# Optimization experiments

Hardware: AMD Instinct MI355X
Metric: run time of the kernel (lower is better)

The kernel has to match this reference:

```python
import jax, jax.numpy as jnp
import numpy as np

EPS = 1e-8  # torch.cosine_similarity default eps


def setup_inputs() -> dict:
    key = jax.random.key(0)
    ks = jax.random.split(key, 6)
    B, U, P, H = 256, 128, 64, 768
    utt_output = jax.random.normal(ks[0], (U, B, H), dtype=jnp.float32)
    pheno_output = jax.random.normal(ks[1], (P, B, H), dtype=jnp.float32)
    # Conv1d(in=U, out=U, kernel=P) weight: [out, in, kernel]
    w_utt = jax.random.normal(ks[2], (U, U, P), dtype=jnp.float32) / np.sqrt(U * P)
    b_utt = jax.random.normal(ks[3], (U,), dtype=jnp.float32) * 0.01
    # Conv1d(in=P, out=P, kernel=U) weight: [out, in, kernel]
    w_pheno = jax.random.normal(ks[4], (P, P, U), dtype=jnp.float32) / np.sqrt(P * U)
    b_pheno = jax.random.normal(ks[5], (P,), dtype=jnp.float32) * 0.01
    return {"utt_output": utt_output, "pheno_output": pheno_output,
            "w_utt": w_utt, "b_utt": b_utt, "w_pheno": w_pheno, "b_pheno": b_pheno}


def reference(utt_output, pheno_output, w_utt, b_utt, w_pheno, b_pheno):
    # [len, B, H] -> [B, len, H]
    u = jnp.swapaxes(utt_output, 0, 1)    # [B, U, H]
    p = jnp.swapaxes(pheno_output, 0, 1)  # [B, P, H]
    # cosine similarity matrix c[b,i,j] = <u_i, p_j> / (max(|u_i|,eps)*max(|p_j|,eps))
    un = u / jnp.maximum(jnp.linalg.norm(u, axis=-1, keepdims=True), EPS)
    pn = p / jnp.maximum(jnp.linalg.norm(p, axis=-1, keepdims=True), EPS)
    c = jnp.einsum('buh,bph->bup', un, pn)  # [B, U, P]
    # Conv1d with kernel covering the full width -> output length 1, i.e. an einsum
    row_logits = jnp.einsum('bup,oup->bo', c, w_utt) + b_utt        # [B, U]
    col_logits = jnp.einsum('bup,opu->bo', c, w_pheno) + b_pheno    # [B, P]
    row_attention = jax.nn.softmax(row_logits, axis=-1)
    col_attention = jax.nn.softmax(col_logits, axis=-1)
    return row_attention, col_attention
```

## Files before the change

### kernel.cpp

```cpp
#include <hip/hip_runtime.h>
#include <stdint.h>

#define Bn 256
#define Un 128
#define Pn 64
#define Hn 768
#define Ototal 192
#define KC 16

#define LDU 40
#define LDB 72

typedef short s4v __attribute__((ext_vector_type(4)));
typedef short s8v __attribute__((ext_vector_type(8)));
typedef float f4v __attribute__((ext_vector_type(4)));

__device__ __forceinline__ short f2bf(float x) {
  union { float f; uint32_t u; } c; c.f = x;
  uint32_t r = (c.u + 0x7fffu + ((c.u >> 16) & 1u)) >> 16;
  return (short)(r & 0xffffu);
}

__device__ __forceinline__ float dot4(float4 v) {
  return v.x * v.x + v.y * v.y + v.z * v.z + v.w * v.w;
}

__global__ void __launch_bounds__(512) phaseAW(const float* __restrict__ utt,
                                               const float* __restrict__ ph,
                                               ushort* __restrict__ Cbf,
                                               const float* __restrict__ w_utt,
                                               const float* __restrict__ w_ph,
                                               ushort* __restrict__ Wbf) {
  __shared__ __align__(16) float smemf[64 * 129];
  char* smem = (char*)smemf;
  const int bx = blockIdx.x;
  const int t = threadIdx.x;

  if (bx >= 512) {
    if (bx < 2560) {
      int idx = (bx - 512) * 512 + t;
      Wbf[idx] = (ushort)f2bf(w_utt[idx]);
      return;
    }
    float* tile = smemf;
    const int oc = bx - 2560;
    const float* src = w_ph + (size_t)oc * 8192;
#pragma unroll
    for (int itr = 0; itr < 4; ++itr) {
      int idx = itr * 2048 + t * 4;
      int j = idx >> 7, i = idx & 127;
      float4 v = *(const float4*)(src + idx);
      tile[j * 129 + i + 0] = v.x;
      tile[j * 129 + i + 1] = v.y;
      tile[j * 129 + i + 2] = v.z;
      tile[j * 129 + i + 3] = v.w;
    }
    __syncthreads();
    const size_t obase = (size_t)(128 + oc) * 8192;
#pragma unroll
    for (int itr = 0; itr < 4; ++itr) {
      int k = itr * 2048 + t * 4;
      int i = k >> 6, j = k & 63;
      s4v o4 = { f2bf(tile[(j + 0) * 129 + i]),
                 f2bf(tile[(j + 1) * 129 + i]),
                 f2bf(tile[(j + 2) * 129 + i]),
                 f2bf(tile[(j + 3) * 129 + i]) };
      *(s4v*)&Wbf[obase + k] = o4;
    }
    return;
  }

  short (*uA)[64 * LDU] = (short (*)[64 * LDU])(smem);
  short (*pB)[64 * LDU] = (short (*)[64 * LDU])(smem + 10240);
  float* s_inu = (float*)(smem + 20480);
  float* s_inp = (float*)(smem + 20736);

  const int b    = (bx & 7) | ((bx >> 4) << 3);
  const int half = (bx >> 3) & 1;
  const int w = t >> 6, l = t & 63;

  const int r  = t >> 3;
  const int cc = (t & 7) * 4;

  const size_t rstride = (size_t)Bn * Hn;
  const float* ubase = utt + (size_t)b * Hn + (size_t)(half * 64 + r) * rstride + cc;
  const float* pbase = ph  + (size_t)b * Hn + (size_t)r * rstride + cc;

  const int m  = l & 15;
  const int ko = (l >> 4) * 8;
  const int it = w & 3;
  const int jp = w >> 2;
  const int lw = r * LDU + (t & 7) * 4;
  const int fo = (it * 16 + m) * LDU + ko;
  const int go = (jp * 32 + m) * LDU + ko;

  f4v zero4 = {0.f, 0.f, 0.f, 0.f};
  f4v acc0 = zero4, acc1 = zero4;
  float ssu = 0.f, ssp = 0.f;

  float4 pu[4], pp[4];
  pu[0] = *(const float4*)(ubase);
  pp[0] = *(const float4*)(pbase);
  pu[1] = *(const float4*)(ubase + 32);
  pp[1] = *(const float4*)(pbase + 32);
  pu[2] = *(const float4*)(ubase + 64);
  pp[2] = *(const float4*)(pbase + 64);
  pu[3] = *(const float4*)(ubase + 96);
  pp[3] = *(const float4*)(pbase + 96);

  {
    float4 a = pu[0], q = pp[0];
    ssu += dot4(a); ssp += dot4(q);
    s4v au = { f2bf(a.x), f2bf(a.y), f2bf(a.z), f2bf(a.w) };
    s4v qq = { f2bf(q.x), f2bf(q.y), f2bf(q.z), f2bf(q.w) };
    *(s4v*)&uA[0][lw] = au;
    *(s4v*)&pB[0][lw] = qq;
  }
  asm volatile("s_waitcnt lgkmcnt(0)" ::: "memory");
  __builtin_amdgcn_s_barrier();
  __builtin_amdgcn_sched_barrier(0);

#pragma unroll
  for (int c = 0; c < 24; ++c) {
    const int cur = c & 1;
    if (c + 4 < 24) {
      pu[(c + 4) & 3] = *(const float4*)(ubase + (c + 4) * 32);
      pp[(c + 4) & 3] = *(const float4*)(pbase + (c + 4) * 32);
    }
    s8v af  = *(const s8v*)&uA[cur][fo];
    s8v bf0 = *(const s8v*)&pB[cur][go];
    s8v bf1 = *(const s8v*)&pB[cur][go + 16 * LDU];
    acc0 = __builtin_amdgcn_mfma_f32_16x16x32_bf16(af, bf0, acc0, 0, 0, 0);
    acc1 = __builtin_amdgcn_mfma_f32_16x16x32_bf16(af, bf1, acc1, 0, 0, 0);
    if (c + 1 < 24) {
      float4 a = pu[(c + 1) & 3], q = pp[(c + 1) & 3];
      ssu += dot4(a); ssp += dot4(q);
      s4v au = { f2bf(a.x), f2bf(a.y), f2bf(a.z), f2bf(a.w) };
      s4v qq = { f2bf(q.x), f2bf(q.y), f2bf(q.z), f2bf(q.w) };
      *(s4v*)&uA[cur ^ 1][lw] = au;
      *(s4v*)&pB[cur ^ 1][lw] = qq;
    }
    asm volatile("s_waitcnt lgkmcnt(0)" ::: "memory");
    __builtin_amdgcn_s_barrier();
    __builtin_amdgcn_sched_barrier(0);
  }

  ssu += __shfl_xor(ssu, 4); ssu += __shfl_xor(ssu, 2); ssu += __shfl_xor(ssu, 1);
  ssp += __shfl_xor(ssp, 4); ssp += __shfl_xor(ssp, 2); ssp += __shfl_xor(ssp, 1);
  if ((t & 7) == 0) {
    s_inu[r] = 1.f / fmaxf(sqrtf(ssu), 1e-8f);
    s_inp[r] = 1.f / fmaxf(sqrtf(ssp), 1e-8f);
  }
  __syncthreads();

  const int cl = l & 15;
  const int rq = (l >> 4) * 4;
#pragma unroll
  for (int jt = 0; jt < 2; ++jt) {
    int j = jp * 32 + jt * 16 + cl;
    float sj = s_inp[j];
    f4v a = (jt == 0) ? acc0 : acc1;
#pragma unroll
    for (int rr = 0; rr < 4; ++rr) {
      int il = it * 16 + rq + rr;
      float v = a[rr] * s_inu[il] * sj;
      Cbf[((size_t)b * Un + half * 64 + il) * Pn + j] = (ushort)f2bf(v);
    }
  }
}

__global__ void __launch_bounds__(256) phaseB(const ushort* __restrict__ Cbf,
                                              const ushort* __restrict__ Wbf,
                                              float* __restrict__ partial) {
  const int kc = blockIdx.x;
  const int mt = blockIdx.y;
  const int nt = blockIdx.z;
  const int t = threadIdx.x;
  const int w = t >> 6, l = t & 63;

  __shared__ short Ab[64 * LDB];
  __shared__ short Bb[64 * LDB];

  const int row = t >> 2;
  const int k16 = (t & 3) * 16;

  f4v zero4 = {0.f, 0.f, 0.f, 0.f};
  f4v acc[4] = {zero4, zero4, zero4, zero4};

  const ushort* Ag = Cbf + (size_t)(mt * 64 + row) * 8192 + kc * 512 + k16;
  const ushort* Bg = Wbf + (size_t)(nt * 64 + row) * 8192 + kc * 512 + k16;
  const int m  = l & 15;
  const int ko = (l >> 4) * 8;

  for (int c = 0; c < 8; ++c) {
    s8v av0 = *(const s8v*)(Ag + c * 64);
    s8v av1 = *(const s8v*)(Ag + c * 64 + 8);
    s8v bv0 = *(const s8v*)(Bg + c * 64);
    s8v bv1 = *(const s8v*)(Bg + c * 64 + 8);
    __syncthreads();
    *(s8v*)&Ab[row * LDB + k16]     = av0;
    *(s8v*)&Ab[row * LDB + k16 + 8] = av1;
    *(s8v*)&Bb[row * LDB + k16]     = bv0;
    *(s8v*)&Bb[row * LDB + k16 + 8] = bv1;
    __syncthreads();
#pragma unroll
    for (int ks = 0; ks < 2; ++ks) {
      s8v af = *(const s8v*)&Ab[(16 * w + m) * LDB + ks * 32 + ko];
#pragma unroll
      for (int jt = 0; jt < 4; ++jt) {
        s8v bf = *(const s8v*)&Bb[(16 * jt + m) * LDB + ks * 32 + ko];
        acc[jt] = __builtin_amdgcn_mfma_f32_16x16x32_bf16(af, bf, acc[jt], 0, 0, 0);
      }
    }
  }

  const int rq = (l >> 4) * 4;
#pragma unroll
  for (int jt = 0; jt < 4; ++jt) {
    int og = nt * 64 + 16 * jt + (l & 15);
#pragma unroll
    for (int r = 0; r < 4; ++r) {
      int bg = mt * 64 + 16 * w + rq + r;
      partial[((size_t)kc * Bn + bg) * Ototal + og] = acc[jt][r];
    }
  }
}

__global__ void __launch_bounds__(192) phaseC(const float* __restrict__ partial,
                                              const float* __restrict__ b_utt,
                                              const float* __restrict__ b_ph,
                                              float* __restrict__ out) {
  const int b = blockIdx.x;
  const int t = threadIdx.x;
  const int w = t >> 6, l = t & 63;

  float v = 0.f;
#pragma unroll
  for (int kc = 0; kc < KC; ++kc)
    v += partial[((size_t)kc * Bn + b) * Ototal + t];
  v += (t < Un) ? b_utt[t] : b_ph[t - Un];

  __shared__ float red[3];
  float mx = v;
  for (int o = 32; o >= 1; o >>= 1) mx = fmaxf(mx, __shfl_xor(mx, o));
  if (l == 0) red[w] = mx;
  __syncthreads();
  float gmax = (t < Un) ? fmaxf(red[0], red[1]) : red[2];
  float e = expf(v - gmax);
  float s = e;
  for (int o = 32; o >= 1; o >>= 1) s += __shfl_xor(s, o);
  __syncthreads();
  if (l == 0) red[w] = s;
  __syncthreads();
  float gs = (t < Un) ? (red[0] + red[1]) : red[2];
  float r = e / gs;
  if (t < Un) out[(size_t)b * Un + t] = r;
  else        out[(size_t)Bn * Un + (size_t)b * Pn + (t - Un)] = r;
}

extern "C" void kernel_launch(void* const* d_in, const int* in_sizes, int n_in,
                              void* d_out, int out_size, void* d_ws, size_t ws_size,
                              hipStream_t stream) {
  const float* utt   = (const float*)d_in[0];
  const float* ph    = (const float*)d_in[1];
  const float* w_utt = (const float*)d_in[2];
  const float* b_utt = (const float*)d_in[3];
  const float* w_ph  = (const float*)d_in[4];
  const float* b_ph  = (const float*)d_in[5];

  char* ws = (char*)d_ws;
  ushort* Cbf     = (ushort*)(ws);
  ushort* Wbf     = (ushort*)(ws + 4194304);
  float*  partial = (float*)(ws + 7340032);

  phaseAW<<<dim3(2624), dim3(512), 0, stream>>>(utt, ph, Cbf, w_utt, w_ph, Wbf);
  phaseB <<<dim3(KC, 4, 3), dim3(256), 0, stream>>>(Cbf, Wbf, partial);
  phaseC <<<dim3(Bn), dim3(192), 0, stream>>>(partial, b_utt, b_ph, (float*)d_out);
}
```

Measured before the change: 213.3 us.

## Stream fp32 tiles via direct global-to-LDS loads with XOR swizzle, convert at fragment read

Replaces the register-staged prefetch (load float4, convert to bf16, write LDS) with global_load_lds async copies of raw fp32 into a double-buffered, XOR-swizzled LDS tile. The bf16 conversion and the norm accumulation move to after the LDS read, just before the MFMA. The goal is to cut VGPR pressure and the register round trip; launch bounds now request 4 waves per EU. The cost is doubled LDS footprint per stage, repeated conversion work, since each element is read by several waves, and a shallower prefetch depth of one stage instead of four.

After: 208.9 us. 1.02x faster.

```diff
diff --git a/kernel.cpp b/kernel.cpp
--- a/kernel.cpp
+++ b/kernel.cpp
@@ -8,7 +8,6 @@
 #define Ototal 192
 #define KC 16
 
-#define LDU 40
 #define LDB 72
 
 typedef short s4v __attribute__((ext_vector_type(4)));
@@ -25,14 +24,26 @@
   return v.x * v.x + v.y * v.y + v.z * v.z + v.w * v.w;
 }
 
-__global__ void __launch_bounds__(512) phaseAW(const float* __restrict__ utt,
-                                               const float* __restrict__ ph,
-                                               ushort* __restrict__ Cbf,
-                                               const float* __restrict__ w_utt,
-                                               const float* __restrict__ w_ph,
-                                               ushort* __restrict__ Wbf) {
-  __shared__ __align__(16) float smemf[64 * 129];
-  char* smem = (char*)smemf;
+__device__ __forceinline__ s8v pack8(float4 x, float4 y) {
+  s8v r;
+  r[0] = f2bf(x.x); r[1] = f2bf(x.y); r[2] = f2bf(x.z); r[3] = f2bf(x.w);
+  r[4] = f2bf(y.x); r[5] = f2bf(y.y); r[6] = f2bf(y.z); r[7] = f2bf(y.w);
+  return r;
+}
+
+__device__ __forceinline__ void gl16(const float* g, float* l) {
+  __builtin_amdgcn_global_load_lds(
+      (const __attribute__((address_space(1))) uint32_t*)g,
+      (__attribute__((address_space(3))) uint32_t*)l, 16, 0, 0);
+}
+
+__global__ void __launch_bounds__(512, 4) phaseAW(const float* __restrict__ utt,
+                                                  const float* __restrict__ ph,
+                                                  ushort* __restrict__ Cbf,
+                                                  const float* __restrict__ w_utt,
+                                                  const float* __restrict__ w_ph,
+                                                  ushort* __restrict__ Wbf) {
+  __shared__ __align__(16) char smem[33280];
   const int bx = blockIdx.x;
   const int t = threadIdx.x;
 
@@ -42,7 +53,7 @@
       Wbf[idx] = (ushort)f2bf(w_utt[idx]);
       return;
     }
-    float* tile = smemf;
+    float* tile = (float*)smem;
     const int oc = bx - 2560;
     const float* src = w_ph + (size_t)oc * 8192;
 #pragma unroll
@@ -70,76 +81,76 @@
     return;
   }
 
-  short (*uA)[64 * LDU] = (short (*)[64 * LDU])(smem);
-  short (*pB)[64 * LDU] = (short (*)[64 * LDU])(smem + 10240);
-  float* s_inu = (float*)(smem + 20480);
-  float* s_inp = (float*)(smem + 20736);
+  float (*uf)[64 * 32] = (float (*)[64 * 32])smem;
+  float (*pf)[64 * 32] = (float (*)[64 * 32])(smem + 16384);
+  float* s_inu = (float*)(smem + 32768);
+  float* s_inp = (float*)(smem + 33024);
 
   const int b    = (bx & 7) | ((bx >> 4) << 3);
   const int half = (bx >> 3) & 1;
   const int w = t >> 6, l = t & 63;
 
-  const int r  = t >> 3;
-  const int cc = (t & 7) * 4;
+  const int r   = t >> 3;
+  const int gsw = (t & 7) ^ (r & 7);
 
   const size_t rstride = (size_t)Bn * Hn;
-  const float* ubase = utt + (size_t)b * Hn + (size_t)(half * 64 + r) * rstride + cc;
-  const float* pbase = ph  + (size_t)b * Hn + (size_t)r * rstride + cc;
+  const float* ubase = utt + (size_t)b * Hn + (size_t)(half * 64 + r) * rstride + gsw * 4;
+  const float* pbase = ph  + (size_t)b * Hn + (size_t)r * rstride + gsw * 4;
+  float* u0d = uf[0] + t * 4;
+  float* u1d = uf[1] + t * 4;
+  float* p0d = pf[0] + t * 4;
+  float* p1d = pf[1] + t * 4;
 
   const int m  = l & 15;
-  const int ko = (l >> 4) * 8;
+  const int g0 = (l >> 4) * 2;
+  const int g1 = g0 + 1;
   const int it = w & 3;
   const int jp = w >> 2;
-  const int lw = r * LDU + (t & 7) * 4;
-  const int fo = (it * 16 + m) * LDU + ko;
-  const int go = (jp * 32 + m) * LDU + ko;
+  const int Ra  = it * 16 + m;
+  const int Rb0 = jp * 32 + m;
+  const int Rb1 = Rb0 + 16;
+  const int sa  = Ra  & 7;
+  const int sb0 = Rb0 & 7;
+  const int sb1 = Rb1 & 7;
 
   f4v zero4 = {0.f, 0.f, 0.f, 0.f};
   f4v acc0 = zero4, acc1 = zero4;
   float ssu = 0.f, ssp = 0.f;
 
-  float4 pu[4], pp[4];
-  pu[0] = *(const float4*)(ubase);
-  pp[0] = *(const float4*)(pbase);
-  pu[1] = *(const float4*)(ubase + 32);
-  pp[1] = *(const float4*)(pbase + 32);
-  pu[2] = *(const float4*)(ubase + 64);
-  pp[2] = *(const float4*)(pbase + 64);
-  pu[3] = *(const float4*)(ubase + 96);
-  pp[3] = *(const float4*)(pbase + 96);
-
-  {
-    float4 a = pu[0], q = pp[0];
-    ssu += dot4(a); ssp += dot4(q);
-    s4v au = { f2bf(a.x), f2bf(a.y), f2bf(a.z), f2bf(a.w) };
-    s4v qq = { f2bf(q.x), f2bf(q.y), f2bf(q.z), f2bf(q.w) };
-    *(s4v*)&uA[0][lw] = au;
-    *(s4v*)&pB[0][lw] = qq;
-  }
-  asm volatile("s_waitcnt lgkmcnt(0)" ::: "memory");
-  __builtin_amdgcn_s_barrier();
-  __builtin_amdgcn_sched_barrier(0);
+  gl16(ubase, u0d);
+  gl16(pbase, p0d);
 
 #pragma unroll
   for (int c = 0; c < 24; ++c) {
-    const int cur = c & 1;
-    if (c + 4 < 24) {
-      pu[(c + 4) & 3] = *(const float4*)(ubase + (c + 4) * 32);
-      pp[(c + 4) & 3] = *(const float4*)(pbase + (c + 4) * 32);
-    }
-    s8v af  = *(const s8v*)&uA[cur][fo];
-    s8v bf0 = *(const s8v*)&pB[cur][go];
-    s8v bf1 = *(const s8v*)&pB[cur][go + 16 * LDU];
+    if (c < 23) {
+      gl16(ubase + (c + 1) * 32, ((c + 1) & 1) ? u1d : u0d);
+      gl16(pbase + (c + 1) * 32, ((c + 1) & 1) ? p1d : p0d);
+      __builtin_amdgcn_sched_barrier(0);
+      asm volatile("s_waitcnt vmcnt(2)" ::: "memory");
+    } else {
+      asm volatile("s_waitcnt vmcnt(0)" ::: "memory");
+    }
+    __builtin_amdgcn_s_barrier();
+    __builtin_amdgcn_sched_barrier(0);
+
+    const float* uB = uf[c & 1];
+    const float* pB = pf[c & 1];
+    float4 fa0  = *(const float4*)(uB + Ra  * 32 + ((g0 ^ sa)  << 2));
+    float4 fa1  = *(const float4*)(uB + Ra  * 32 + ((g1 ^ sa)  << 2));
+    float4 fb00 = *(const float4*)(pB + Rb0 * 32 + ((g0 ^ sb0) << 2));
+    float4 fb01 = *(const float4*)(pB + Rb0 * 32 + ((g1 ^ sb0) << 2));
+    float4 fb10 = *(const float4*)(pB + Rb1 * 32 + ((g0 ^ sb1) << 2));
+    float4 fb11 = *(const float4*)(pB + Rb1 * 32 + ((g1 ^ sb1) << 2));
+    float4 su = *(const float4*)(uB + t * 4);
+    float4 sp = *(const float4*)(pB + t * 4);
+    ssu += dot4(su);
+    ssp += dot4(sp);
+    s8v af  = pack8(fa0, fa1);
+    s8v bf0 = pack8(fb00, fb01);
+    s8v bf1 = pack8(fb10, fb11);
     acc0 = __builtin_amdgcn_mfma_f32_16x16x32_bf16(af, bf0, acc0, 0, 0, 0);
     acc1 = __builtin_amdgcn_mfma_f32_16x16x32_bf16(af, bf1, acc1, 0, 0, 0);
-    if (c + 1 < 24) {
-      float4 a = pu[(c + 1) & 3], q = pp[(c + 1) & 3];
-      ssu += dot4(a); ssp += dot4(q);
-      s4v au = { f2bf(a.x), f2bf(a.y), f2bf(a.z), f2bf(a.w) };
-      s4v qq = { f2bf(q.x), f2bf(q.y), f2bf(q.z), f2bf(q.w) };
-      *(s4v*)&uA[cur ^ 1][lw] = au;
-      *(s4v*)&pB[cur ^ 1][lw] = qq;
-    }
+
     asm volatile("s_waitcnt lgkmcnt(0)" ::: "memory");
     __builtin_amdgcn_s_barrier();
     __builtin_amdgcn_sched_barrier(0);
```
